# Kernel tuning notes

Hardware: AMD Instinct MI355X
Metric: run time of the kernel (lower is better)

The kernel has to match this reference:

```python
import jax, jax.numpy as jnp
import numpy as np
from jax import lax

C = 32    # feats_channels
CT = 16   # transform_channels
B, D, H, W = 1, 16, 16, 32  # N = D*H*W = 8192


def _bcast(v):
    return v[None, :, None, None, None]


def conv1(x, w):
    # 1x1x1 Conv3d, no bias: w [O, I], x [b, I, d, h, w]
    return jnp.einsum('oi,bidhw->bodhw', w, x)


def cbr(x, w, s, b):
    # Conv1x1x1 + inference BatchNorm (folded to scale s / bias b) + ReLU
    return jax.nn.relu(conv1(x, w) * _bcast(s) + _bcast(b))


def setup_inputs() -> dict:
    key = jax.random.key(0)
    ks = jax.random.split(key, 16)

    def wmat(k, shape, scale=0.05):
        return jax.random.normal(k, shape, jnp.float32) * scale

    def bn(k, n):
        k1, k2 = jax.random.split(k)
        s = 1.0 + 0.05 * jax.random.normal(k1, (n,), jnp.float32)
        b = 0.05 * jax.random.normal(k2, (n,), jnp.float32)
        return s, b

    inp = {'x': jax.random.normal(ks[0], (B, C, D, H, W), jnp.float32)}
    # query_project: 2 convs (C->CT, CT->CT), each conv+BN+ReLU
    inp['wq1'] = wmat(ks[1], (CT, C));  inp['sq1'], inp['bq1'] = bn(ks[2], CT)
    inp['wq2'] = wmat(ks[3], (CT, CT)); inp['sq2'], inp['bq2'] = bn(ks[4], CT)
    # key_project: 2 convs (2C->CT, CT->CT)
    inp['wk1'] = wmat(ks[5], (CT, 2 * C)); inp['sk1'], inp['bk1'] = bn(ks[6], CT)
    inp['wk2'] = wmat(ks[7], (CT, CT));    inp['sk2'], inp['bk2'] = bn(ks[8], CT)
    # value_project: 1 conv (2C->CT) + BN + ReLU
    inp['wv'] = wmat(ks[9], (CT, 2 * C)); inp['sv'], inp['bv'] = bn(ks[10], CT)
    # out_project: 1 conv (CT->C) + BN + ReLU
    inp['wo'] = wmat(ks[11], (C, CT)); inp['so'], inp['bo'] = bn(ks[12], C)
    # bottleneck: Conv3d(2C->C, k=3, pad=1, no bias) + BN + LeakyReLU(0.1)
    inp['wbot'] = wmat(ks[13], (C, 2 * C, 3, 3, 3), 0.02)
    inp['sbot'], inp['bbot'] = bn(ks[14], C)
    return inp


def reference(x, wq1, sq1, bq1, wq2, sq2, bq2,
              wk1, sk1, bk1, wk2, sk2, bk2,
              wv, sv, bv, wo, so, bo, wbot, sbot, bbot):
    b, c, d, h, w = x.shape
    # AdaptiveAvgPool2d((1,1)) on (b, c*d, h, w) = mean over (h, w) per (c,d);
    # bilinear upsample from 1x1 is a constant broadcast.
    xg = jnp.mean(x, axis=(3, 4), keepdims=True)
    key_feats = jnp.concatenate([jnp.broadcast_to(xg, x.shape), x], axis=1)  # [b, 2c, d, h, w]

    q = cbr(cbr(x, wq1, sq1, bq1), wq2, sq2, bq2)          # [b, CT, d, h, w]
    k = cbr(cbr(key_feats, wk1, sk1, bk1), wk2, sk2, bk2)  # [b, CT, d, h, w]
    v = cbr(key_feats, wv, sv, bv)                          # [b, CT, d, h, w]

    n = d * h * w
    q = q.reshape(b, CT, n).transpose(0, 2, 1)  # [b, N, CT]
    k = k.reshape(b, CT, n)                     # [b, CT, N]
    v = v.reshape(b, CT, n).transpose(0, 2, 1)  # [b, N, CT]

    sim = jnp.einsum('bnc,bcm->bnm', q, k) * (CT ** -0.5)   # [b, N, N]
    sim = jax.nn.softmax(sim, axis=-1)
    ctx = jnp.einsum('bnm,bmc->bnc', sim, v)                # [b, N, CT]
    ctx = ctx.transpose(0, 2, 1).reshape(b, CT, d, h, w)
    ctx = cbr(ctx, wo, so, bo)                              # [b, C, d, h, w]

    fused = jnp.concatenate([x, ctx], axis=1)               # [b, 2C, d, h, w]
    y = lax.conv_general_dilated(
        fused, wbot, window_strides=(1, 1, 1), padding='SAME',
        dimension_numbers=('NCDHW', 'OIDHW', 'NCDHW'))
    y = y * _bcast(sbot) + _bcast(bbot)
    return jnp.where(y > 0, y, 0.1 * y)  # LeakyReLU(0.1)
```

## Files before the change

kernel.cpp:

```cpp
#include <hip/hip_runtime.h>

typedef unsigned int u32;
typedef unsigned short u16;
typedef float f32x16 __attribute__((ext_vector_type(16)));
typedef __bf16 bf16x8 __attribute__((ext_vector_type(8)));
union BF8 { u32 w[4]; bf16x8 v; };

#define DEVI static __device__ __forceinline__
DEVI u32 pk_bf16(float lo, float hi) {
  u32 r;
  asm("v_cvt_pk_bf16_f32 %0, %1, %2" : "=v"(r) : "v"(lo), "v"(hi));
  return r;
}
DEVI u16 bf1(float x) { return (u16)(pk_bf16(x, 0.0f) & 0xffffu); }

#define WB_WREP  0
#define WB_QS    131072
#define WB_K     393216
#define WB_VT    655360
#define WB_FUS   917504

__global__ __launch_bounds__(256) void k_prep(
    const float* __restrict__ x,
    const float* __restrict__ wq1, const float* __restrict__ sq1, const float* __restrict__ bq1,
    const float* __restrict__ wq2, const float* __restrict__ sq2, const float* __restrict__ bq2,
    const float* __restrict__ wk1, const float* __restrict__ sk1, const float* __restrict__ bk1,
    const float* __restrict__ wk2, const float* __restrict__ sk2, const float* __restrict__ bk2,
    const float* __restrict__ wv,  const float* __restrict__ sv,  const float* __restrict__ bv,
    const float* __restrict__ wbot, const float* __restrict__ sbot,
    u16* __restrict__ qs, u16* __restrict__ kbm, u16* __restrict__ vt,
    u16* __restrict__ fus, u16* __restrict__ wrep) {
  const int tid = threadIdx.x;
  const int bid = blockIdx.x;
  if (bid >= 256) {
    const int rb = bid - 256;
#pragma unroll
    for (int e = 0; e < 8; ++e) {
      const int idx = rb * 2048 + tid * 8 + e;
      const int tap = idx >> 11, rem = idx & 2047, o = rem >> 6, i = rem & 63;
      wrep[idx] = bf1(wbot[(o * 64 + i) * 27 + tap] * sbot[o]);
    }
    return;
  }
  __shared__ float H[2][32][17];
  __shared__ float P8[32][8];
  __shared__ float xgs[32];
  const int n0 = bid << 5;
  const int d = n0 >> 9;
  {
    const int c = tid >> 3, part = tid & 7;
    const float4* xp = (const float4*)(x + (c << 13) + (d << 9));
    float s = 0.f;
#pragma unroll
    for (int i = 0; i < 16; ++i) {
      const float4 v4 = xp[part + (i << 3)];
      s += v4.x + v4.y + v4.z + v4.w;
    }
    P8[c][part] = s;
  }
  __syncthreads();
  if (tid < 32) {
    float s = 0.f;
#pragma unroll
    for (int j = 0; j < 8; ++j) s += P8[tid][j];
    xgs[tid] = s * (1.0f / 512.0f);
  }
  __syncthreads();
  const int nl = tid & 31, g = tid >> 5;
  const int n = n0 + nl;
  const int r0 = 2 * g, r1 = r0 + 1;
  float xr[32], xgv[32];
#pragma unroll
  for (int c = 0; c < 32; ++c) xr[c] = x[(c << 13) + n];
#pragma unroll
  for (int c = 0; c < 32; ++c) xgv[c] = xgs[c];

  const float4* wq1f = (const float4*)wq1;
  const float4* wk1f = (const float4*)wk1;
  const float4* wvf  = (const float4*)wv;
  float dq0 = 0.f, dq1 = 0.f, dk0 = 0.f, dk1 = 0.f, dv0 = 0.f, dv1 = 0.f;
#pragma unroll
  for (int c4 = 0; c4 < 8; ++c4) {
    const float4 wa = wq1f[r0 * 8 + c4], wb = wq1f[r1 * 8 + c4];
    dq0 += wa.x * xr[4*c4+0] + wa.y * xr[4*c4+1] + wa.z * xr[4*c4+2] + wa.w * xr[4*c4+3];
    dq1 += wb.x * xr[4*c4+0] + wb.y * xr[4*c4+1] + wb.z * xr[4*c4+2] + wb.w * xr[4*c4+3];
  }
#pragma unroll
  for (int c4 = 0; c4 < 8; ++c4) {
    const float4 ka = wk1f[r0 * 16 + c4], kb = wk1f[r1 * 16 + c4];
    dk0 += ka.x * xgv[4*c4+0] + ka.y * xgv[4*c4+1] + ka.z * xgv[4*c4+2] + ka.w * xgv[4*c4+3];
    dk1 += kb.x * xgv[4*c4+0] + kb.y * xgv[4*c4+1] + kb.z * xgv[4*c4+2] + kb.w * xgv[4*c4+3];
    const float4 va = wvf[r0 * 16 + c4], vb = wvf[r1 * 16 + c4];
    dv0 += va.x * xgv[4*c4+0] + va.y * xgv[4*c4+1] + va.z * xgv[4*c4+2] + va.w * xgv[4*c4+3];
    dv1 += vb.x * xgv[4*c4+0] + vb.y * xgv[4*c4+1] + vb.z * xgv[4*c4+2] + vb.w * xgv[4*c4+3];
  }
#pragma unroll
  for (int c4 = 0; c4 < 8; ++c4) {
    const float4 ka = wk1f[r0 * 16 + 8 + c4], kb = wk1f[r1 * 16 + 8 + c4];
    dk0 += ka.x * xr[4*c4+0] + ka.y * xr[4*c4+1] + ka.z * xr[4*c4+2] + ka.w * xr[4*c4+3];
    dk1 += kb.x * xr[4*c4+0] + kb.y * xr[4*c4+1] + kb.z * xr[4*c4+2] + kb.w * xr[4*c4+3];
    const float4 va = wvf[r0 * 16 + 8 + c4], vb = wvf[r1 * 16 + 8 + c4];
    dv0 += va.x * xr[4*c4+0] + va.y * xr[4*c4+1] + va.z * xr[4*c4+2] + va.w * xr[4*c4+3];
    dv1 += vb.x * xr[4*c4+0] + vb.y * xr[4*c4+1] + vb.z * xr[4*c4+2] + vb.w * xr[4*c4+3];
  }
  const float hq0 = fmaxf(dq0 * sq1[r0] + bq1[r0], 0.f);
  const float hq1 = fmaxf(dq1 * sq1[r1] + bq1[r1], 0.f);
  const float hk0 = fmaxf(dk0 * sk1[r0] + bk1[r0], 0.f);
  const float hk1 = fmaxf(dk1 * sk1[r1] + bk1[r1], 0.f);
  const float hv0 = fmaxf(dv0 * sv[r0] + bv[r0], 0.f);
  const float hv1 = fmaxf(dv1 * sv[r1] + bv[r1], 0.f);
  H[0][nl][r0] = hq0; H[0][nl][r1] = hq1;
  H[1][nl][r0] = hk0; H[1][nl][r1] = hk1;
  vt[(r0 << 13) + n] = bf1(hv0);
  vt[(r1 << 13) + n] = bf1(hv1);
  const int c0 = g << 2;
  *(u32*)(fus + (n << 6) + c0)     = pk_bf16(xr[c0],     xr[c0 + 1]);
  *(u32*)(fus + (n << 6) + c0 + 2) = pk_bf16(xr[c0 + 2], xr[c0 + 3]);
  __syncthreads();

  float eq0 = 0.f, eq1 = 0.f, ek0 = 0.f, ek1 = 0.f;
#pragma unroll
  for (int j = 0; j < 16; ++j) {
    const float hq = H[0][nl][j], hk = H[1][nl][j];
    eq0 += wq2[r0 * 16 + j] * hq;
    eq1 += wq2[r1 * 16 + j] * hq;
    ek0 += wk2[r0 * 16 + j] * hk;
    ek1 += wk2[r1 * 16 + j] * hk;
  }
  const float SC = 0.36067376022224085f;
  const float q0 = fmaxf(eq0 * (sq2[r0] * SC) + bq2[r0] * SC, 0.f);
  const float q1 = fmaxf(eq1 * (sq2[r1] * SC) + bq2[r1] * SC, 0.f);
  const float k0 = fmaxf(ek0 * sk2[r0] + bk2[r0], 0.f);
  const float k1 = fmaxf(ek1 * sk2[r1] + bk2[r1], 0.f);
  *(u32*)(qs  + (n << 4) + r0) = pk_bf16(q0, q1);
  *(u32*)(kbm + (n << 4) + r0) = pk_bf16(k0, k1);
}

__global__ __launch_bounds__(1024) void k_attn(
    const u16* __restrict__ qs, const u16* __restrict__ kbm, const u16* __restrict__ vt,
    const float* __restrict__ wo, const float* __restrict__ so, const float* __restrict__ bo,
    u16* __restrict__ fus) {
  __shared__ float R[16][32][17];
  const int tid = threadIdx.x;
  const int w = tid >> 6, lane = tid & 63;
  const int l31 = lane & 31, h = lane >> 5;
  const int qb = blockIdx.x;

  const bf16x8 qf = *(const bf16x8*)(qs + (((qb << 5) + l31) << 4) + (h << 3));
  f32x16 acc_a, acc_b, z;
#pragma unroll
  for (int i = 0; i < 16; ++i) { acc_a[i] = 0.f; acc_b[i] = 0.f; z[i] = 0.f; }

  const u32 fill = (l31 == 16) ? 0x3F803F80u : 0u;
  const int kb0 = w << 9;
  const bool vlane = (l31 < 16);
  const u16* vrow = vt + (l31 << 13) + (h << 3);

  bf16x8 kf_c = *(const bf16x8*)(kbm + ((kb0 + l31) << 4) + (h << 3));
  BF8 V1c, V2c;
#pragma unroll
  for (int j2 = 0; j2 < 4; ++j2) { V1c.w[j2] = fill; V2c.w[j2] = fill; }
  if (vlane) {
    V1c.v = *(const bf16x8*)(vrow + kb0);
    V2c.v = *(const bf16x8*)(vrow + kb0 + 16);
  }

#pragma unroll
  for (int t = 0; t < 16; ++t) {
    const bf16x8 kf = kf_c;
    const BF8 V1 = V1c, V2 = V2c;
    if (t < 15) {
      const int kbn = kb0 + ((t + 1) << 5);
      kf_c = *(const bf16x8*)(kbm + ((kbn + l31) << 4) + (h << 3));
      if (vlane) {
        V1c.v = *(const bf16x8*)(vrow + kbn);
        V2c.v = *(const bf16x8*)(vrow + kbn + 16);
      }
    }
    const f32x16 st = __builtin_amdgcn_mfma_f32_32x32x16_bf16(kf, qf, z, 0, 0, 0);
    float pe[16];
#pragma unroll
    for (int r = 0; r < 16; ++r) pe[r] = __builtin_amdgcn_exp2f(st[r]);
    u32 a0 = pk_bf16(pe[0],  pe[1]),  a1 = pk_bf16(pe[2],  pe[3]);
    u32 a2 = pk_bf16(pe[4],  pe[5]),  a3 = pk_bf16(pe[6],  pe[7]);
    u32 b0 = pk_bf16(pe[8],  pe[9]),  b1 = pk_bf16(pe[10], pe[11]);
    u32 b2 = pk_bf16(pe[12], pe[13]), b3 = pk_bf16(pe[14], pe[15]);
    asm("v_permlane32_swap_b32 %0, %1" : "+v"(a0), "+v"(a2));
    asm("v_permlane32_swap_b32 %0, %1" : "+v"(a1), "+v"(a3));
    asm("v_permlane32_swap_b32 %0, %1" : "+v"(b0), "+v"(b2));
    asm("v_permlane32_swap_b32 %0, %1" : "+v"(b1), "+v"(b3));
    BF8 A1, A2;
    A1.w[0] = a0; A1.w[1] = a1; A1.w[2] = a2; A1.w[3] = a3;
    A2.w[0] = b0; A2.w[1] = b1; A2.w[2] = b2; A2.w[3] = b3;
    __builtin_amdgcn_s_setprio(1);
    acc_a = __builtin_amdgcn_mfma_f32_32x32x16_bf16(A1.v, V1.v, acc_a, 0, 0, 0);
    acc_b = __builtin_amdgcn_mfma_f32_32x32x16_bf16(A2.v, V2.v, acc_b, 0, 0, 0);
    __builtin_amdgcn_s_setprio(0);
  }
  if (l31 < 17) {
#pragma unroll
    for (int r = 0; r < 16; ++r) {
      const int row = (r & 3) + ((r >> 2) << 3) + (h << 2);
      R[w][row][l31] = acc_a[r] + acc_b[r];
    }
  }
  __syncthreads();
  float* Rf = &R[0][0][0];
  if (tid < 544) {
    float s0 = 0.f;
#pragma unroll
    for (int w2 = 0; w2 < 16; ++w2) s0 += Rf[w2 * 544 + tid];
    Rf[tid] = s0;
  }
  __syncthreads();
  if (tid < 512) {
    const int row = tid >> 4;
    const int o0 = (tid & 15) << 1, o1 = o0 + 1;
    const float inv = 1.0f / Rf[row * 17 + 16];
    float d0 = 0.f, d1 = 0.f;
#pragma unroll
    for (int c = 0; c < 16; ++c) {
      const float cv = Rf[row * 17 + c];
      d0 += wo[o0 * 16 + c] * cv;
      d1 += wo[o1 * 16 + c] * cv;
    }
    const float y0 = fmaxf(bo[o0] + so[o0] * d0 * inv, 0.f);
    const float y1 = fmaxf(bo[o1] + so[o1] * d1 * inv, 0.f);
    *(u32*)(fus + (((qb << 5) + row) << 6) + 32 + o0) = pk_bf16(y0, y1);
  }
}

__global__ __launch_bounds__(512) void k_conv(
    const u16* __restrict__ fus, const u16* __restrict__ wrep,
    const float* __restrict__ bbot, float* __restrict__ out) {
  __shared__ float R8[8][1024];
  const int tid = threadIdx.x;
  const int wv = tid >> 6, lane = tid & 63;
  const int l31 = lane & 31, h = lane >> 5;
  const int n0 = blockIdx.x << 5;
  const int dz = n0 >> 9, hy = (n0 >> 5) & 15;
  f32x16 acc0, acc1;
#pragma unroll
  for (int i = 0; i < 16; ++i) { acc0[i] = 0.f; acc1[i] = 0.f; }
  const int ulo = (wv * 54) >> 3, uhi = ((wv + 1) * 54) >> 3;

  const u16* bp_c; const u16* wp_c; bool ok_c;
  {
    const int tap = ulo >> 1, ch = (ulo & 1) << 1;
    const int dd = tap / 9 - 1, dh = (tap / 3) % 3 - 1, dw = tap % 3 - 1;
    ok_c = ((unsigned)(dz + dd) < 16u) & ((unsigned)(hy + dh) < 16u) &
           ((unsigned)(l31 + dw) < 32u);
    const int nn = n0 + dd * 512 + dh * 32 + dw + l31;
    bp_c = fus + (nn << 6) + (ch << 4) + (h << 3);
    wp_c = wrep + ((tap * 32 + l31) << 6) + (ch << 4) + (h << 3);
  }
  BF8 B0c, B1c;
  B0c.w[0] = B0c.w[1] = B0c.w[2] = B0c.w[3] = 0u;
  B1c.w[0] = B1c.w[1] = B1c.w[2] = B1c.w[3] = 0u;
  if (ok_c) { B0c.v = *(const bf16x8*)bp_c; B1c.v = *(const bf16x8*)(bp_c + 16); }

  for (int u = ulo; u < uhi; ++u) {
    const BF8 B0 = B0c, B1 = B1c;
    const u16* wp = wp_c;
    if (u + 1 < uhi) {
      const int un = u + 1;
      const int tap = un >> 1, ch = (un & 1) << 1;
      const int dd = tap / 9 - 1, dh = (tap / 3) % 3 - 1, dw = tap % 3 - 1;
      const bool ok = ((unsigned)(dz + dd) < 16u) & ((unsigned)(hy + dh) < 16u) &
                      ((unsigned)(l31 + dw) < 32u);
      const int nn = n0 + dd * 512 + dh * 32 + dw + l31;
      const u16* bp = fus + (nn << 6) + (ch << 4) + (h << 3);
      wp_c = wrep + ((tap * 32 + l31) << 6) + (ch << 4) + (h << 3);
      B0c.w[0] = B0c.w[1] = B0c.w[2] = B0c.w[3] = 0u;
      B1c.w[0] = B1c.w[1] = B1c.w[2] = B1c.w[3] = 0u;
      if (ok) { B0c.v = *(const bf16x8*)bp; B1c.v = *(const bf16x8*)(bp + 16); }
    }
    const bf16x8 af0 = *(const bf16x8*)wp;
    const bf16x8 af1 = *(const bf16x8*)(wp + 16);
    __builtin_amdgcn_s_setprio(1);
    acc0 = __builtin_amdgcn_mfma_f32_32x32x16_bf16(af0, B0.v, acc0, 0, 0, 0);
    acc1 = __builtin_amdgcn_mfma_f32_32x32x16_bf16(af1, B1.v, acc1, 0, 0, 0);
    __builtin_amdgcn_s_setprio(0);
  }
#pragma unroll
  for (int r = 0; r < 16; ++r) {
    const int row = (r & 3) + ((r >> 2) << 3) + (h << 2);
    R8[wv][(row << 5) + l31] = acc0[r] + acc1[r];
  }
  __syncthreads();
#pragma unroll
  for (int k2 = 0; k2 < 2; ++k2) {
    const int e = tid + (k2 << 9);
    const int row = e >> 5;
    float yv = bbot[row];
#pragma unroll
    for (int w2 = 0; w2 < 8; ++w2) yv += R8[w2][e];
    out[(row << 13) + n0 + (e & 31)] = yv > 0.f ? yv : 0.1f * yv;
  }
}

extern "C" void kernel_launch(void* const* d_in, const int* in_sizes, int n_in,
                              void* d_out, int out_size, void* d_ws, size_t ws_size,
                              hipStream_t stream) {
  const float* x    = (const float*)d_in[0];
  const float* wq1  = (const float*)d_in[1];
  const float* sq1  = (const float*)d_in[2];
  const float* bq1  = (const float*)d_in[3];
  const float* wq2  = (const float*)d_in[4];
  const float* sq2  = (const float*)d_in[5];
  const float* bq2  = (const float*)d_in[6];
  const float* wk1  = (const float*)d_in[7];
  const float* sk1  = (const float*)d_in[8];
  const float* bk1  = (const float*)d_in[9];
  const float* wk2  = (const float*)d_in[10];
  const float* sk2  = (const float*)d_in[11];
  const float* bk2  = (const float*)d_in[12];
  const float* wv   = (const float*)d_in[13];
  const float* sv   = (const float*)d_in[14];
  const float* bv   = (const float*)d_in[15];
  const float* wo   = (const float*)d_in[16];
  const float* so   = (const float*)d_in[17];
  const float* bo   = (const float*)d_in[18];
  const float* wbot = (const float*)d_in[19];
  const float* sbot = (const float*)d_in[20];
  const float* bbot = (const float*)d_in[21];
  (void)in_sizes; (void)n_in; (void)out_size; (void)ws_size;

  char* wsb = (char*)d_ws;
  u16* wrep = (u16*)(wsb + WB_WREP);
  u16* qs   = (u16*)(wsb + WB_QS);
  u16* kbm  = (u16*)(wsb + WB_K);
  u16* vt   = (u16*)(wsb + WB_VT);
  u16* fus  = (u16*)(wsb + WB_FUS);
  float* out = (float*)d_out;

  k_prep<<<283, 256, 0, stream>>>(x, wq1, sq1, bq1, wq2, sq2, bq2,
                                  wk1, sk1, bk1, wk2, sk2, bk2,
                                  wv, sv, bv, wbot, sbot,
                                  qs, kbm, vt, fus, wrep);
  k_attn<<<256, 1024, 0, stream>>>(qs, kbm, vt, wo, so, bo, fus);
  k_conv<<<256, 512, 0, stream>>>(fus, wrep, bbot, out);
}
```

Before: 35.90 us.

## Fuse prep, attention and conv into one cooperative kernel with grid syncs

Merges the three separate launches (prep, attention, bottleneck conv) into one cooperative kernel of 256 blocks x 1024 threads, with grid.sync() between phases. The aim is to remove launch gaps and per-kernel ramp-up/drain between stages. The conv phase now splits its 54 tap-chunks across 16 waves instead of 8, and the weight repacking is spread across all blocks. In exchange, the prep phase leaves 3/4 of the threads idle, and cooperative grid barriers carry their own cost and depend on all 256 blocks being co-resident.

```diff
diff --git a/kernel.cpp b/kernel.cpp
--- a/kernel.cpp
+++ b/kernel.cpp
@@ -1,4 +1,7 @@
 #include <hip/hip_runtime.h>
+#include <hip/hip_cooperative_groups.h>
+
+namespace cg = cooperative_groups;
 
 typedef unsigned int u32;
 typedef unsigned short u16;
@@ -20,324 +23,316 @@
 #define WB_VT    655360
 #define WB_FUS   917504
 
-__global__ __launch_bounds__(256) void k_prep(
-    const float* __restrict__ x,
-    const float* __restrict__ wq1, const float* __restrict__ sq1, const float* __restrict__ bq1,
-    const float* __restrict__ wq2, const float* __restrict__ sq2, const float* __restrict__ bq2,
-    const float* __restrict__ wk1, const float* __restrict__ sk1, const float* __restrict__ bk1,
-    const float* __restrict__ wk2, const float* __restrict__ sk2, const float* __restrict__ bk2,
-    const float* __restrict__ wv,  const float* __restrict__ sv,  const float* __restrict__ bv,
-    const float* __restrict__ wbot, const float* __restrict__ sbot,
-    u16* __restrict__ qs, u16* __restrict__ kbm, u16* __restrict__ vt,
-    u16* __restrict__ fus, u16* __restrict__ wrep) {
+struct Params {
+  const float *x;
+  const float *wq1, *sq1, *bq1, *wq2, *sq2, *bq2;
+  const float *wk1, *sk1, *bk1, *wk2, *sk2, *bk2;
+  const float *wv, *sv, *bv, *wo, *so, *bo;
+  const float *wbot, *sbot, *bbot;
+  u16 *qs, *kbm, *vt, *fus, *wrep;
+  float *out;
+};
+
+__global__ __launch_bounds__(1024) void k_fused(Params p) {
+  __shared__ float SH[16384];
   const int tid = threadIdx.x;
   const int bid = blockIdx.x;
-  if (bid >= 256) {
-    const int rb = bid - 256;
-#pragma unroll
-    for (int e = 0; e < 8; ++e) {
-      const int idx = rb * 2048 + tid * 8 + e;
+  const int n0 = bid << 5;
+  cg::grid_group grid = cg::this_grid();
+
+  {
+    if (tid < 256) {
+      const int d = n0 >> 9;
+      const int c = tid >> 3, part = tid & 7;
+      const float4* xp = (const float4*)(p.x + (c << 13) + (d << 9));
+      float s = 0.f;
+#pragma unroll
+      for (int i = 0; i < 16; ++i) {
+        const float4 v4 = xp[part + (i << 3)];
+        s += v4.x + v4.y + v4.z + v4.w;
+      }
+      SH[1088 + (c << 3) + part] = s;
+    }
+    if (tid >= 256 && tid < 472) {
+      const int idx = bid * 216 + (tid - 256);
       const int tap = idx >> 11, rem = idx & 2047, o = rem >> 6, i = rem & 63;
-      wrep[idx] = bf1(wbot[(o * 64 + i) * 27 + tap] * sbot[o]);
-    }
-    return;
+      p.wrep[idx] = bf1(p.wbot[(o * 64 + i) * 27 + tap] * p.sbot[o]);
+    }
+    __syncthreads();
+    if (tid < 32) {
+      float s = 0.f;
+#pragma unroll
+      for (int j = 0; j < 8; ++j) s += SH[1088 + (tid << 3) + j];
+      SH[1344 + tid] = s * (1.0f / 512.0f);
+    }
+    __syncthreads();
+    if (tid < 256) {
+      const int nl = tid & 31, g = tid >> 5;
+      const int n = n0 + nl;
+      const int r0 = 2 * g, r1 = r0 + 1;
+      float xr[32], xgv[32];
+#pragma unroll
+      for (int c = 0; c < 32; ++c) xr[c] = p.x[(c << 13) + n];
+#pragma unroll
+      for (int c = 0; c < 32; ++c) xgv[c] = SH[1344 + c];
+
+      const float4* wq1f = (const float4*)p.wq1;
+      const float4* wk1f = (const float4*)p.wk1;
+      const float4* wvf  = (const float4*)p.wv;
+      float dq0 = 0.f, dq1 = 0.f, dk0 = 0.f, dk1 = 0.f, dv0 = 0.f, dv1 = 0.f;
+#pragma unroll
+      for (int c4 = 0; c4 < 8; ++c4) {
+        const float4 wa = wq1f[r0 * 8 + c4], wb = wq1f[r1 * 8 + c4];
+        dq0 += wa.x * xr[4*c4+0] + wa.y * xr[4*c4+1] + wa.z * xr[4*c4+2] + wa.w * xr[4*c4+3];
+        dq1 += wb.x * xr[4*c4+0] + wb.y * xr[4*c4+1] + wb.z * xr[4*c4+2] + wb.w * xr[4*c4+3];
+      }
+#pragma unroll
+      for (int c4 = 0; c4 < 8; ++c4) {
+        const float4 ka = wk1f[r0 * 16 + c4], kb = wk1f[r1 * 16 + c4];
+        dk0 += ka.x * xgv[4*c4+0] + ka.y * xgv[4*c4+1] + ka.z * xgv[4*c4+2] + ka.w * xgv[4*c4+3];
+        dk1 += kb.x * xgv[4*c4+0] + kb.y * xgv[4*c4+1] + kb.z * xgv[4*c4+2] + kb.w * xgv[4*c4+3];
+        const float4 va = wvf[r0 * 16 + c4], vb = wvf[r1 * 16 + c4];
+        dv0 += va.x * xgv[4*c4+0] + va.y * xgv[4*c4+1] + va.z * xgv[4*c4+2] + va.w * xgv[4*c4+3];
+        dv1 += vb.x * xgv[4*c4+0] + vb.y * xgv[4*c4+1] + vb.z * xgv[4*c4+2] + vb.w * xgv[4*c4+3];
+      }
+#pragma unroll
+      for (int c4 = 0; c4 < 8; ++c4) {
+        const float4 ka = wk1f[r0 * 16 + 8 + c4], kb = wk1f[r1 * 16 + 8 + c4];
+        dk0 += ka.x * xr[4*c4+0] + ka.y * xr[4*c4+1] + ka.z * xr[4*c4+2] + ka.w * xr[4*c4+3];
+        dk1 += kb.x * xr[4*c4+0] + kb.y * xr[4*c4+1] + kb.z * xr[4*c4+2] + kb.w * xr[4*c4+3];
+        const float4 va = wvf[r0 * 16 + 8 + c4], vb = wvf[r1 * 16 + 8 + c4];
+        dv0 += va.x * xr[4*c4+0] + va.y * xr[4*c4+1] + va.z * xr[4*c4+2] + va.w * xr[4*c4+3];
+        dv1 += vb.x * xr[4*c4+0] + vb.y * xr[4*c4+1] + vb.z * xr[4*c4+2] + vb.w * xr[4*c4+3];
+      }
+      const float hq0 = fmaxf(dq0 * p.sq1[r0] + p.bq1[r0], 0.f);
+      const float hq1 = fmaxf(dq1 * p.sq1[r1] + p.bq1[r1], 0.f);
+      const float hk0 = fmaxf(dk0 * p.sk1[r0] + p.bk1[r0], 0.f);
+      const float hk1 = fmaxf(dk1 * p.sk1[r1] + p.bk1[r1], 0.f);
+      const float hv0 = fmaxf(dv0 * p.sv[r0] + p.bv[r0], 0.f);
+      const float hv1 = fmaxf(dv1 * p.sv[r1] + p.bv[r1], 0.f);
+      SH[nl * 17 + r0] = hq0;       SH[nl * 17 + r1] = hq1;
+      SH[544 + nl * 17 + r0] = hk0; SH[544 + nl * 17 + r1] = hk1;
+      p.vt[(r0 << 13) + n] = bf1(hv0);
+      p.vt[(r1 << 13) + n] = bf1(hv1);
+      const int c0 = g << 2;
+      *(u32*)(p.fus + (n << 6) + c0)     = pk_bf16(xr[c0],     xr[c0 + 1]);
+      *(u32*)(p.fus + (n << 6) + c0 + 2) = pk_bf16(xr[c0 + 2], xr[c0 + 3]);
+    }
+    __syncthreads();
+    if (tid < 256) {
+      const int nl = tid & 31, g = tid >> 5;
+      const int n = n0 + nl;
+      const int r0 = 2 * g, r1 = r0 + 1;
+      float eq0 = 0.f, eq1 = 0.f, ek0 = 0.f, ek1 = 0.f;
+#pragma unroll
+      for (int j = 0; j < 16; ++j) {
+        const float hq = SH[nl * 17 + j], hk = SH[544 + nl * 17 + j];
+        eq0 += p.wq2[r0 * 16 + j] * hq;
+        eq1 += p.wq2[r1 * 16 + j] * hq;
+        ek0 += p.wk2[r0 * 16 + j] * hk;
+        ek1 += p.wk2[r1 * 16 + j] * hk;
+      }
+      const float SC = 0.36067376022224085f;
+      const float q0 = fmaxf(eq0 * (p.sq2[r0] * SC) + p.bq2[r0] * SC, 0.f);
+      const float q1 = fmaxf(eq1 * (p.sq2[r1] * SC) + p.bq2[r1] * SC, 0.f);
+      const float k0 = fmaxf(ek0 * p.sk2[r0] + p.bk2[r0], 0.f);
+      const float k1 = fmaxf(ek1 * p.sk2[r1] + p.bk2[r1], 0.f);
+      *(u32*)(p.qs  + (n << 4) + r0) = pk_bf16(q0, q1);
+      *(u32*)(p.kbm + (n << 4) + r0) = pk_bf16(k0, k1);
+    }
   }
-  __shared__ float H[2][32][17];
-  __shared__ float P8[32][8];
-  __shared__ float xgs[32];
-  const int n0 = bid << 5;
-  const int d = n0 >> 9;
+
+  grid.sync();
+
   {
-    const int c = tid >> 3, part = tid & 7;
-    const float4* xp = (const float4*)(x + (c << 13) + (d << 9));
-    float s = 0.f;
-#pragma unroll
-    for (int i = 0; i < 16; ++i) {
-      const float4 v4 = xp[part + (i << 3)];
-      s += v4.x + v4.y + v4.z + v4.w;
-    }
-    P8[c][part] = s;
+    const int w = tid >> 6, lane = tid & 63;
+    const int l31 = lane & 31, h = lane >> 5;
+    const int qb = bid;
+
+    const bf16x8 qf = *(const bf16x8*)(p.qs + (((qb << 5) + l31) << 4) + (h << 3));
+    f32x16 acc_a, acc_b, z;
+#pragma unroll
+    for (int i = 0; i < 16; ++i) { acc_a[i] = 0.f; acc_b[i] = 0.f; z[i] = 0.f; }
+
+    const u32 fill = (l31 == 16) ? 0x3F803F80u : 0u;
+    const int kb0 = w << 9;
+    const bool vlane = (l31 < 16);
+    const u16* vrow = p.vt + (l31 << 13) + (h << 3);
+
+    bf16x8 kf_c = *(const bf16x8*)(p.kbm + ((kb0 + l31) << 4) + (h << 3));
+    BF8 V1c, V2c;
+#pragma unroll
+    for (int j2 = 0; j2 < 4; ++j2) { V1c.w[j2] = fill; V2c.w[j2] = fill; }
+    if (vlane) {
+      V1c.v = *(const bf16x8*)(vrow + kb0);
+      V2c.v = *(const bf16x8*)(vrow + kb0 + 16);
+    }
+
+#pragma unroll
+    for (int t = 0; t < 16; ++t) {
+      const bf16x8 kf = kf_c;
+      const BF8 V1 = V1c, V2 = V2c;
+      if (t < 15) {
+        const int kbn = kb0 + ((t + 1) << 5);
+        kf_c = *(const bf16x8*)(p.kbm + ((kbn + l31) << 4) + (h << 3));
+        if (vlane) {
+          V1c.v = *(const bf16x8*)(vrow + kbn);
+          V2c.v = *(const bf16x8*)(vrow + kbn + 16);
+        }
+      }
+      const f32x16 st = __builtin_amdgcn_mfma_f32_32x32x16_bf16(kf, qf, z, 0, 0, 0);
+      float pe[16];
+#pragma unroll
+      for (int r = 0; r < 16; ++r) pe[r] = __builtin_amdgcn_exp2f(st[r]);
+      u32 a0 = pk_bf16(pe[0],  pe[1]),  a1 = pk_bf16(pe[2],  pe[3]);
+      u32 a2 = pk_bf16(pe[4],  pe[5]),  a3 = pk_bf16(pe[6],  pe[7]);
+      u32 b0 = pk_bf16(pe[8],  pe[9]),  b1 = pk_bf16(pe[10], pe[11]);
+      u32 b2 = pk_bf16(pe[12], pe[13]), b3 = pk_bf16(pe[14], pe[15]);
+      asm("v_permlane32_swap_b32 %0, %1" : "+v"(a0), "+v"(a2));
+      asm("v_permlane32_swap_b32 %0, %1" : "+v"(a1), "+v"(a3));
+      asm("v_permlane32_swap_b32 %0, %1" : "+v"(b0), "+v"(b2));
+      asm("v_permlane32_swap_b32 %0, %1" : "+v"(b1), "+v"(b3));
+      BF8 A1, A2;
+      A1.w[0] = a0; A1.w[1] = a1; A1.w[2] = a2; A1.w[3] = a3;
+      A2.w[0] = b0; A2.w[1] = b1; A2.w[2] = b2; A2.w[3] = b3;
+      __builtin_amdgcn_s_setprio(1);
+      acc_a = __builtin_amdgcn_mfma_f32_32x32x16_bf16(A1.v, V1.v, acc_a, 0, 0, 0);
+      acc_b = __builtin_amdgcn_mfma_f32_32x32x16_bf16(A2.v, V2.v, acc_b, 0, 0, 0);
+      __builtin_amdgcn_s_setprio(0);
+    }
+    if (l31 < 17) {
+#pragma unroll
+      for (int r = 0; r < 16; ++r) {
+        const int row = (r & 3) + ((r >> 2) << 3) + (h << 2);
+        SH[w * 544 + row * 17 + l31] = acc_a[r] + acc_b[r];
+      }
+    }
+    __syncthreads();
+    if (tid < 544) {
+      float s0 = 0.f;
+#pragma unroll
+      for (int w2 = 0; w2 < 16; ++w2) s0 += SH[w2 * 544 + tid];
+      SH[tid] = s0;
+    }
+    __syncthreads();
+    if (tid < 512) {
+      const int row = tid >> 4;
+      const int o0 = (tid & 15) << 1, o1 = o0 + 1;
+      const float inv = 1.0f / SH[row * 17 + 16];
+      float d0 = 0.f, d1 = 0.f;
+#pragma unroll
+      for (int c = 0; c < 16; ++c) {
+        const float cv = SH[row * 17 + c];
+        d0 += p.wo[o0 * 16 + c] * cv;
+        d1 += p.wo[o1 * 16 + c] * cv;
+      }
+      const float y0 = fmaxf(p.bo[o0] + p.so[o0] * d0 * inv, 0.f);
+      const float y1 = fmaxf(p.bo[o1] + p.so[o1] * d1 * inv, 0.f);
+      *(u32*)(p.fus + (((qb << 5) + row) << 6) + 32 + o0) = pk_bf16(y0, y1);
+    }
   }
-  __syncthreads();
-  if (tid < 32) {
-    float s = 0.f;
-#pragma unroll
-    for (int j = 0; j < 8; ++j) s += P8[tid][j];
-    xgs[tid] = s * (1.0f / 512.0f);
-  }
-  __syncthreads();
-  const int nl = tid & 31, g = tid >> 5;
-  const int n = n0 + nl;
-  const int r0 = 2 * g, r1 = r0 + 1;
-  float xr[32], xgv[32];
-#pragma unroll
-  for (int c = 0; c < 32; ++c) xr[c] = x[(c << 13) + n];
-#pragma unroll
-  for (int c = 0; c < 32; ++c) xgv[c] = xgs[c];
-
-  const float4* wq1f = (const float4*)wq1;
-  const float4* wk1f = (const float4*)wk1;
-  const float4* wvf  = (const float4*)wv;
-  float dq0 = 0.f, dq1 = 0.f, dk0 = 0.f, dk1 = 0.f, dv0 = 0.f, dv1 = 0.f;
-#pragma unroll
-  for (int c4 = 0; c4 < 8; ++c4) {
-    const float4 wa = wq1f[r0 * 8 + c4], wb = wq1f[r1 * 8 + c4];
-    dq0 += wa.x * xr[4*c4+0] + wa.y * xr[4*c4+1] + wa.z * xr[4*c4+2] + wa.w * xr[4*c4+3];
-    dq1 += wb.x * xr[4*c4+0] + wb.y * xr[4*c4+1] + wb.z * xr[4*c4+2] + wb.w * xr[4*c4+3];
-  }
-#pragma unroll
-  for (int c4 = 0; c4 < 8; ++c4) {
-    const float4 ka = wk1f[r0 * 16 + c4], kb = wk1f[r1 * 16 + c4];
-    dk0 += ka.x * xgv[4*c4+0] + ka.y * xgv[4*c4+1] + ka.z * xgv[4*c4+2] + ka.w * xgv[4*c4+3];
-    dk1 += kb.x * xgv[4*c4+0] + kb.y * xgv[4*c4+1] + kb.z * xgv[4*c4+2] + kb.w * xgv[4*c4+3];
-    const float4 va = wvf[r0 * 16 + c4], vb = wvf[r1 * 16 + c4];
-    dv0 += va.x * xgv[4*c4+0] + va.y * xgv[4*c4+1] + va.z * xgv[4*c4+2] + va.w * xgv[4*c4+3];
-    dv1 += vb.x * xgv[4*c4+0] + vb.y * xgv[4*c4+1] + vb.z * xgv[4*c4+2] + vb.w * xgv[4*c4+3];
-  }
-#pragma unroll
-  for (int c4 = 0; c4 < 8; ++c4) {
-    const float4 ka = wk1f[r0 * 16 + 8 + c4], kb = wk1f[r1 * 16 + 8 + c4];
-    dk0 += ka.x * xr[4*c4+0] + ka.y * xr[4*c4+1] + ka.z * xr[4*c4+2] + ka.w * xr[4*c4+3];
-    dk1 += kb.x * xr[4*c4+0] + kb.y * xr[4*c4+1] + kb.z * xr[4*c4+2] + kb.w * xr[4*c4+3];
-    const float4 va = wvf[r0 * 16 + 8 + c4], vb = wvf[r1 * 16 + 8 + c4];
-    dv0 += va.x * xr[4*c4+0] + va.y * xr[4*c4+1] + va.z * xr[4*c4+2] + va.w * xr[4*c4+3];
-    dv1 += vb.x * xr[4*c4+0] + vb.y * xr[4*c4+1] + vb.z * xr[4*c4+2] + vb.w * xr[4*c4+3];
-  }
-  const float hq0 = fmaxf(dq0 * sq1[r0] + bq1[r0], 0.f);
-  const float hq1 = fmaxf(dq1 * sq1[r1] + bq1[r1], 0.f);
-  const float hk0 = fmaxf(dk0 * sk1[r0] + bk1[r0], 0.f);
-  const float hk1 = fmaxf(dk1 * sk1[r1] + bk1[r1], 0.f);
-  const float hv0 = fmaxf(dv0 * sv[r0] + bv[r0], 0.f);
-  const float hv1 = fmaxf(dv1 * sv[r1] + bv[r1], 0.f);
-  H[0][nl][r0] = hq0; H[0][nl][r1] = hq1;
-  H[1][nl][r0] = hk0; H[1][nl][r1] = hk1;
-  vt[(r0 << 13) + n] = bf1(hv0);
-  vt[(r1 << 13) + n] = bf1(hv1);
-  const int c0 = g << 2;
-  *(u32*)(fus + (n << 6) + c0)     = pk_bf16(xr[c0],     xr[c0 + 1]);
-  *(u32*)(fus + (n << 6) + c0 + 2) = pk_bf16(xr[c0 + 2], xr[c0 + 3]);
-  __syncthreads();
-
-  float eq0 = 0.f, eq1 = 0.f, ek0 = 0.f, ek1 = 0.f;
-#pragma unroll
-  for (int j = 0; j < 16; ++j) {
-    const float hq = H[0][nl][j], hk = H[1][nl][j];
-    eq0 += wq2[r0 * 16 + j] * hq;
-    eq1 += wq2[r1 * 16 + j] * hq;
-    ek0 += wk2[r0 * 16 + j] * hk;
-    ek1 += wk2[r1 * 16 + j] * hk;
-  }
-  const float SC = 0.36067376022224085f;
-  const float q0 = fmaxf(eq0 * (sq2[r0] * SC) + bq2[r0] * SC, 0.f);
-  const float q1 = fmaxf(eq1 * (sq2[r1] * SC) + bq2[r1] * SC, 0.f);
-  const float k0 = fmaxf(ek0 * sk2[r0] + bk2[r0], 0.f);
-  const float k1 = fmaxf(ek1 * sk2[r1] + bk2[r1], 0.f);
-  *(u32*)(qs  + (n << 4) + r0) = pk_bf16(q0, q1);
-  *(u32*)(kbm + (n << 4) + r0) = pk_bf16(k0, k1);
-}
-
-__global__ __launch_bounds__(1024) void k_attn(
-    const u16* __restrict__ qs, const u16* __restrict__ kbm, const u16* __restrict__ vt,
-    const float* __restrict__ wo, const float* __restrict__ so, const float* __restrict__ bo,
-    u16* __restrict__ fus) {
-  __shared__ float R[16][32][17];
-  const int tid = threadIdx.x;
-  const int w = tid >> 6, lane = tid & 63;
-  const int l31 = lane & 31, h = lane >> 5;
-  const int qb = blockIdx.x;
-
-  const bf16x8 qf = *(const bf16x8*)(qs + (((qb << 5) + l31) << 4) + (h << 3));
-  f32x16 acc_a, acc_b, z;
-#pragma unroll
-  for (int i = 0; i < 16; ++i) { acc_a[i] = 0.f; acc_b[i] = 0.f; z[i] = 0.f; }
-
-  const u32 fill = (l31 == 16) ? 0x3F803F80u : 0u;
-  const int kb0 = w << 9;
-  const bool vlane = (l31 < 16);
-  const u16* vrow = vt + (l31 << 13) + (h << 3);
-
-  bf16x8 kf_c = *(const bf16x8*)(kbm + ((kb0 + l31) << 4) + (h << 3));
-  BF8 V1c, V2c;
-#pragma unroll
-  for (int j2 = 0; j2 < 4; ++j2) { V1c.w[j2] = fill; V2c.w[j2] = fill; }
-  if (vlane) {
-    V1c.v = *(const bf16x8*)(vrow + kb0);
-    V2c.v = *(const bf16x8*)(vrow + kb0 + 16);
-  }
-
-#pragma unroll
-  for (int t = 0; t < 16; ++t) {
-    const bf16x8 kf = kf_c;
-    const BF8 V1 = V1c, V2 = V2c;
-    if (t < 15) {
-      const int kbn = kb0 + ((t + 1) << 5);
-      kf_c = *(const bf16x8*)(kbm + ((kbn + l31) << 4) + (h << 3));
-      if (vlane) {
-        V1c.v = *(const bf16x8*)(vrow + kbn);
-        V2c.v = *(const bf16x8*)(vrow + kbn + 16);
-      }
-    }
-    const f32x16 st = __builtin_amdgcn_mfma_f32_32x32x16_bf16(kf, qf, z, 0, 0, 0);
-    float pe[16];
-#pragma unroll
-    for (int r = 0; r < 16; ++r) pe[r] = __builtin_amdgcn_exp2f(st[r]);
-    u32 a0 = pk_bf16(pe[0],  pe[1]),  a1 = pk_bf16(pe[2],  pe[3]);
-    u32 a2 = pk_bf16(pe[4],  pe[5]),  a3 = pk_bf16(pe[6],  pe[7]);
-    u32 b0 = pk_bf16(pe[8],  pe[9]),  b1 = pk_bf16(pe[10], pe[11]);
-    u32 b2 = pk_bf16(pe[12], pe[13]), b3 = pk_bf16(pe[14], pe[15]);
-    asm("v_permlane32_swap_b32 %0, %1" : "+v"(a0), "+v"(a2));
-    asm("v_permlane32_swap_b32 %0, %1" : "+v"(a1), "+v"(a3));
-    asm("v_permlane32_swap_b32 %0, %1" : "+v"(b0), "+v"(b2));
-    asm("v_permlane32_swap_b32 %0, %1" : "+v"(b1), "+v"(b3));
-    BF8 A1, A2;
-    A1.w[0] = a0; A1.w[1] = a1; A1.w[2] = a2; A1.w[3] = a3;
-    A2.w[0] = b0; A2.w[1] = b1; A2.w[2] = b2; A2.w[3] = b3;
-    __builtin_amdgcn_s_setprio(1);
-    acc_a = __builtin_amdgcn_mfma_f32_32x32x16_bf16(A1.v, V1.v, acc_a, 0, 0, 0);
-    acc_b = __builtin_amdgcn_mfma_f32_32x32x16_bf16(A2.v, V2.v, acc_b, 0, 0, 0);
-    __builtin_amdgcn_s_setprio(0);
-  }
-  if (l31 < 17) {
+
+  grid.sync();
+
+  {
+    const int wv = tid >> 6, lane = tid & 63;
+    const int l31 = lane & 31, h = lane >> 5;
+    const int dz = n0 >> 9, hy = (n0 >> 5) & 15;
+    f32x16 acc0, acc1;
+#pragma unroll
+    for (int i = 0; i < 16; ++i) { acc0[i] = 0.f; acc1[i] = 0.f; }
+    const int ulo = (wv * 54) >> 4, uhi = ((wv + 1) * 54) >> 4;
+
+    const u16* bp_c; const u16* wp_c; bool ok_c;
+    {
+      const int tap = ulo >> 1, ch = (ulo & 1) << 1;
+      const int dd = tap / 9 - 1, dh = (tap / 3) % 3 - 1, dw = tap % 3 - 1;
+      ok_c = ((unsigned)(dz + dd) < 16u) & ((unsigned)(hy + dh) < 16u) &
+             ((unsigned)(l31 + dw) < 32u);
+      const int nn = n0 + dd * 512 + dh * 32 + dw + l31;
+      bp_c = p.fus + (nn << 6) + (ch << 4) + (h << 3);
+      wp_c = p.wrep + ((tap * 32 + l31) << 6) + (ch << 4) + (h << 3);
+    }
+    BF8 B0c, B1c;
+    B0c.w[0] = B0c.w[1] = B0c.w[2] = B0c.w[3] = 0u;
+    B1c.w[0] = B1c.w[1] = B1c.w[2] = B1c.w[3] = 0u;
+    if (ok_c) { B0c.v = *(const bf16x8*)bp_c; B1c.v = *(const bf16x8*)(bp_c + 16); }
+
+    for (int u = ulo; u < uhi; ++u) {
+      const BF8 B0 = B0c, B1 = B1c;
+      const u16* wp = wp_c;
+      if (u + 1 < uhi) {
+        const int un = u + 1;
+        const int tap = un >> 1, ch = (un & 1) << 1;
+        const int dd = tap / 9 - 1, dh = (tap / 3) % 3 - 1, dw = tap % 3 - 1;
+        const bool ok = ((unsigned)(dz + dd) < 16u) & ((unsigned)(hy + dh) < 16u) &
+                        ((unsigned)(l31 + dw) < 32u);
+        const int nn = n0 + dd * 512 + dh * 32 + dw + l31;
+        const u16* bp = p.fus + (nn << 6) + (ch << 4) + (h << 3);
+        wp_c = p.wrep + ((tap * 32 + l31) << 6) + (ch << 4) + (h << 3);
+        B0c.w[0] = B0c.w[1] = B0c.w[2] = B0c.w[3] = 0u;
+        B1c.w[0] = B1c.w[1] = B1c.w[2] = B1c.w[3] = 0u;
+        if (ok) { B0c.v = *(const bf16x8*)bp; B1c.v = *(const bf16x8*)(bp + 16); }
+      }
+      const bf16x8 af0 = *(const bf16x8*)wp;
+      const bf16x8 af1 = *(const bf16x8*)(wp + 16);
+      __builtin_amdgcn_s_setprio(1);
+      acc0 = __builtin_amdgcn_mfma_f32_32x32x16_bf16(af0, B0.v, acc0, 0, 0, 0);
+      acc1 = __builtin_amdgcn_mfma_f32_32x32x16_bf16(af1, B1.v, acc1, 0, 0, 0);
+      __builtin_amdgcn_s_setprio(0);
+    }
 #pragma unroll
     for (int r = 0; r < 16; ++r) {
       const int row = (r & 3) + ((r >> 2) << 3) + (h << 2);
-      R[w][row][l31] = acc_a[r] + acc_b[r];
-    }
-  }
-  __syncthreads();
-  float* Rf = &R[0][0][0];
-  if (tid < 544) {
-    float s0 = 0.f;
-#pragma unroll
-    for (int w2 = 0; w2 < 16; ++w2) s0 += Rf[w2 * 544 + tid];
-    Rf[tid] = s0;
-  }
-  __syncthreads();
-  if (tid < 512) {
-    const int row = tid >> 4;
-    const int o0 = (tid & 15) << 1, o1 = o0 + 1;
-    const float inv = 1.0f / Rf[row * 17 + 16];
-    float d0 = 0.f, d1 = 0.f;
-#pragma unroll
-    for (int c = 0; c < 16; ++c) {
-      const float cv = Rf[row * 17 + c];
-      d0 += wo[o0 * 16 + c] * cv;
-      d1 += wo[o1 * 16 + c] * cv;
-    }
-    const float y0 = fmaxf(bo[o0] + so[o0] * d0 * inv, 0.f);
-    const float y1 = fmaxf(bo[o1] + so[o1] * d1 * inv, 0.f);
-    *(u32*)(fus + (((qb << 5) + row) << 6) + 32 + o0) = pk_bf16(y0, y1);
-  }
-}
-
-__global__ __launch_bounds__(512) void k_conv(
-    const u16* __restrict__ fus, const u16* __restrict__ wrep,
-    const float* __restrict__ bbot, float* __restrict__ out) {
-  __shared__ float R8[8][1024];
-  const int tid = threadIdx.x;
-  const int wv = tid >> 6, lane = tid & 63;
-  const int l31 = lane & 31, h = lane >> 5;
-  const int n0 = blockIdx.x << 5;
-  const int dz = n0 >> 9, hy = (n0 >> 5) & 15;
-  f32x16 acc0, acc1;
-#pragma unroll
-  for (int i = 0; i < 16; ++i) { acc0[i] = 0.f; acc1[i] = 0.f; }
-  const int ulo = (wv * 54) >> 3, uhi = ((wv + 1) * 54) >> 3;
-
-  const u16* bp_c; const u16* wp_c; bool ok_c;
-  {
-    const int tap = ulo >> 1, ch = (ulo & 1) << 1;
-    const int dd = tap / 9 - 1, dh = (tap / 3) % 3 - 1, dw = tap % 3 - 1;
-    ok_c = ((unsigned)(dz + dd) < 16u) & ((unsigned)(hy + dh) < 16u) &
-           ((unsigned)(l31 + dw) < 32u);
-    const int nn = n0 + dd * 512 + dh * 32 + dw + l31;
-    bp_c = fus + (nn << 6) + (ch << 4) + (h << 3);
-    wp_c = wrep + ((tap * 32 + l31) << 6) + (ch << 4) + (h << 3);
-  }
-  BF8 B0c, B1c;
-  B0c.w[0] = B0c.w[1] = B0c.w[2] = B0c.w[3] = 0u;
-  B1c.w[0] = B1c.w[1] = B1c.w[2] = B1c.w[3] = 0u;
-  if (ok_c) { B0c.v = *(const bf16x8*)bp_c; B1c.v = *(const bf16x8*)(bp_c + 16); }
-
-  for (int u = ulo; u < uhi; ++u) {
-    const BF8 B0 = B0c, B1 = B1c;
-    const u16* wp = wp_c;
-    if (u + 1 < uhi) {
-      const int un = u + 1;
-      const int tap = un >> 1, ch = (un & 1) << 1;
-      const int dd = tap / 9 - 1, dh = (tap / 3) % 3 - 1, dw = tap % 3 - 1;
-      const bool ok = ((unsigned)(dz + dd) < 16u) & ((unsigned)(hy + dh) < 16u) &
-                      ((unsigned)(l31 + dw) < 32u);
-      const int nn = n0 + dd * 512 + dh * 32 + dw + l31;
-      const u16* bp = fus + (nn << 6) + (ch << 4) + (h << 3);
-      wp_c = wrep + ((tap * 32 + l31) << 6) + (ch << 4) + (h << 3);
-      B0c.w[0] = B0c.w[1] = B0c.w[2] = B0c.w[3] = 0u;
-      B1c.w[0] = B1c.w[1] = B1c.w[2] = B1c.w[3] = 0u;
-      if (ok) { B0c.v = *(const bf16x8*)bp; B1c.v = *(const bf16x8*)(bp + 16); }
-    }
-    const bf16x8 af0 = *(const bf16x8*)wp;
-    const bf16x8 af1 = *(const bf16x8*)(wp + 16);
-    __builtin_amdgcn_s_setprio(1);
-    acc0 = __builtin_amdgcn_mfma_f32_32x32x16_bf16(af0, B0.v, acc0, 0, 0, 0);
-    acc1 = __builtin_amdgcn_mfma_f32_32x32x16_bf16(af1, B1.v, acc1, 0, 0, 0);
-    __builtin_amdgcn_s_setprio(0);
-  }
-#pragma unroll
-  for (int r = 0; r < 16; ++r) {
-    const int row = (r & 3) + ((r >> 2) << 3) + (h << 2);
-    R8[wv][(row << 5) + l31] = acc0[r] + acc1[r];
-  }
-  __syncthreads();
-#pragma unroll
-  for (int k2 = 0; k2 < 2; ++k2) {
-    const int e = tid + (k2 << 9);
-    const int row = e >> 5;
-    float yv = bbot[row];
-#pragma unroll
-    for (int w2 = 0; w2 < 8; ++w2) yv += R8[w2][e];
-    out[(row << 13) + n0 + (e & 31)] = yv > 0.f ? yv : 0.1f * yv;
+      SH[wv * 1024 + (row << 5) + l31] = acc0[r] + acc1[r];
+    }
+    __syncthreads();
+    {
+      const int row = tid >> 5;
+      float yv = p.bbot[row];
+#pragma unroll
+      for (int w2 = 0; w2 < 16; ++w2) yv += SH[w2 * 1024 + tid];
+      p.out[(row << 13) + n0 + (tid & 31)] = yv > 0.f ? yv : 0.1f * yv;
+    }
   }
 }
 
 extern "C" void kernel_launch(void* const* d_in, const int* in_sizes, int n_in,
                               void* d_out, int out_size, void* d_ws, size_t ws_size,
                               hipStream_t stream) {
-  const float* x    = (const float*)d_in[0];
-  const float* wq1  = (const float*)d_in[1];
-  const float* sq1  = (const float*)d_in[2];
-  const float* bq1  = (const float*)d_in[3];
-  const float* wq2  = (const float*)d_in[4];
-  const float* sq2  = (const float*)d_in[5];
-  const float* bq2  = (const float*)d_in[6];
-  const float* wk1  = (const float*)d_in[7];
-  const float* sk1  = (const float*)d_in[8];
-  const float* bk1  = (const float*)d_in[9];
-  const float* wk2  = (const float*)d_in[10];
-  const float* sk2  = (const float*)d_in[11];
-  const float* bk2  = (const float*)d_in[12];
-  const float* wv   = (const float*)d_in[13];
-  const float* sv   = (const float*)d_in[14];
-  const float* bv   = (const float*)d_in[15];
-  const float* wo   = (const float*)d_in[16];
-  const float* so   = (const float*)d_in[17];
-  const float* bo   = (const float*)d_in[18];
-  const float* wbot = (const float*)d_in[19];
-  const float* sbot = (const float*)d_in[20];
-  const float* bbot = (const float*)d_in[21];
   (void)in_sizes; (void)n_in; (void)out_size; (void)ws_size;
-
   char* wsb = (char*)d_ws;
-  u16* wrep = (u16*)(wsb + WB_WREP);
-  u16* qs   = (u16*)(wsb + WB_QS);
-  u16* kbm  = (u16*)(wsb + WB_K);
-  u16* vt   = (u16*)(wsb + WB_VT);
-  u16* fus  = (u16*)(wsb + WB_FUS);
-  float* out = (float*)d_out;
-
-  k_prep<<<283, 256, 0, stream>>>(x, wq1, sq1, bq1, wq2, sq2, bq2,
-                                  wk1, sk1, bk1, wk2, sk2, bk2,
-                                  wv, sv, bv, wbot, sbot,
-                                  qs, kbm, vt, fus, wrep);
-  k_attn<<<256, 1024, 0, stream>>>(qs, kbm, vt, wo, so, bo, fus);
-  k_conv<<<256, 512, 0, stream>>>(fus, wrep, bbot, out);
+  Params hp;
+  hp.x    = (const float*)d_in[0];
+  hp.wq1  = (const float*)d_in[1];
+  hp.sq1  = (const float*)d_in[2];
+  hp.bq1  = (const float*)d_in[3];
+  hp.wq2  = (const float*)d_in[4];
+  hp.sq2  = (const float*)d_in[5];
+  hp.bq2  = (const float*)d_in[6];
+  hp.wk1  = (const float*)d_in[7];
+  hp.sk1  = (const float*)d_in[8];
+  hp.bk1  = (const float*)d_in[9];
+  hp.wk2  = (const float*)d_in[10];
+  hp.sk2  = (const float*)d_in[11];
+  hp.bk2  = (const float*)d_in[12];
+  hp.wv   = (const float*)d_in[13];
+  hp.sv   = (const float*)d_in[14];
+  hp.bv   = (const float*)d_in[15];
+  hp.wo   = (const float*)d_in[16];
+  hp.so   = (const float*)d_in[17];
+  hp.bo   = (const float*)d_in[18];
+  hp.wbot = (const float*)d_in[19];
+  hp.sbot = (const float*)d_in[20];
+  hp.bbot = (const float*)d_in[21];
+  hp.qs   = (u16*)(wsb + WB_QS);
+  hp.kbm  = (u16*)(wsb + WB_K);
+  hp.vt   = (u16*)(wsb + WB_VT);
+  hp.fus  = (u16*)(wsb + WB_FUS);
+  hp.wrep = (u16*)(wsb + WB_WREP);
+  hp.out  = (float*)d_out;
+
+  void* kargs[] = { &hp };
+  hipLaunchCooperativeKernel((const void*)k_fused, dim3(256), dim3(1024),
+                             kargs, 0, stream);
 }
```

Result: slower. 105.9 us (+195.0%).
